# Optimization experiments

Hardware: AMD Instinct MI355X
Metric: run time of the kernel (lower is better)

The kernel has to match this reference:

```python
import jax, jax.numpy as jnp
import numpy as np

WS = 11
SIGMA = 1.5
L = 1.0  # val_range


def _gaussian_window(ws=WS, sigma=SIGMA):
    x = np.arange(ws, dtype=np.float64) - ws // 2
    g = np.exp(-(x ** 2) / (2.0 * sigma ** 2))
    g = g / g.sum()
    w2d = np.outer(g, g)
    return jnp.asarray(w2d, dtype=jnp.float32)  # [ws, ws]


def _depthwise_blur(x, w2d):
    # x: [B, C, H, W]; depthwise gaussian conv with SAME-style padding ws//2
    c = x.shape[1]
    kern = jnp.broadcast_to(w2d, (c, 1, WS, WS)).astype(x.dtype)  # OIHW, groups=C
    pad = WS // 2
    return jax.lax.conv_general_dilated(
        x, kern, window_strides=(1, 1), padding=[(pad, pad), (pad, pad)],
        dimension_numbers=('NCHW', 'OIHW', 'NCHW'), feature_group_count=c)


def setup_inputs() -> dict:
    key = jax.random.key(0)
    k1, k2 = jax.random.split(key)
    img1 = jax.random.uniform(k1, (32, 3, 512, 512), dtype=jnp.float32)
    img2 = jax.random.uniform(k2, (32, 3, 512, 512), dtype=jnp.float32)
    return {"img1": img1, "img2": img2}


def reference(img1, img2):
    w2d = _gaussian_window()
    mu1 = _depthwise_blur(img1, w2d)
    mu2 = _depthwise_blur(img2, w2d)
    mu1_sq = mu1 * mu1
    mu2_sq = mu2 * mu2
    mu1_mu2 = mu1 * mu2
    sigma1_sq = _depthwise_blur(img1 * img1, w2d) - mu1_sq
    sigma2_sq = _depthwise_blur(img2 * img2, w2d) - mu2_sq
    sigma12 = _depthwise_blur(img1 * img2, w2d) - mu1_mu2
    C1 = (0.01 * L) ** 2
    C2 = (0.03 * L) ** 2
    ssim_map = ((2.0 * mu1_mu2 + C1) * (2.0 * sigma12 + C2)) / (
        (mu1_sq + mu2_sq + C1) * (sigma1_sq + sigma2_sq + C2))
    return 1.0 - ssim_map.mean()
```

## Files before the change

kernel.cpp:

```cpp
#include <hip/hip_runtime.h>
#include <math.h>

typedef _Float16 f16;
typedef _Float16 f16x8 __attribute__((ext_vector_type(8)));
typedef _Float16 f16x4 __attribute__((ext_vector_type(4)));
typedef float f32x4 __attribute__((ext_vector_type(4)));

#define ROWS 88
#define NTHREADS 256

__device__ __forceinline__ float ssim_px(float m1, float m2, float mss, float m12) {
  const float C1 = 0.0001f, C2 = 0.0009f;
  const float mu1s = m1 * m1, mu2s = m2 * m2, mu12 = m1 * m2;
  const float num = (2.f * mu12 + C1) * (2.f * (m12 - mu12) + C2);
  const float den = (mu1s + mu2s + C1) * (mss - mu1s - mu2s + C2);
  return num * __builtin_amdgcn_rcpf(den);
}

__device__ __forceinline__ void h_phase(
    const float* __restrict__ p1, const float* __restrict__ p2,
    f16 (*si)[64][ROWS], bool masked,
    int gy0, int xb, int px, int n, int kg, const f16x8& Bh)
{
#pragma unroll
  for (int rg = 0; rg < 5; rg++) {
    const int rimg = gy0 + rg * 16 + n;
    float okf;
    size_t base;
    if (masked) {
      const bool octok = (xb >= 0) && (xb <= 504);
      const bool rok = (rimg >= 0) && (rimg < 512);
      okf = (rok && octok) ? 1.f : 0.f;
      const int rc = rok ? rimg : 0;
      const int xc = octok ? xb : 0;
      base = ((size_t)rc << 9) + (size_t)xc;
    } else {
      okf = 1.f;
      base = ((size_t)rimg << 9) + (size_t)xb;
    }
    const float4 a0 = *(const float4*)(p1 + base);
    const float4 a1 = *(const float4*)(p1 + base + 4);
    const float4 b0 = *(const float4*)(p2 + base);
    const float4 b1 = *(const float4*)(p2 + base + 4);
    const float av[8] = {a0.x, a0.y, a0.z, a0.w, a1.x, a1.y, a1.z, a1.w};
    const float bw[8] = {b0.x, b0.y, b0.z, b0.w, b1.x, b1.y, b1.z, b1.w};
    f16x8 fa, fb, fs, fp;
#pragma unroll
    for (int i = 0; i < 8; i++) {
      float ai = av[i], bi = bw[i];
      if (masked) { ai *= okf; bi *= okf; }
      fa[i] = (f16)ai;
      fb[i] = (f16)bi;
      fs[i] = (f16)fmaf(ai, ai, bi * bi);
      fp[i] = (f16)(ai * bi);
    }
    const f32x4 z = {0.f, 0.f, 0.f, 0.f};
    const f32x4 Da = __builtin_amdgcn_mfma_f32_16x16x32_f16(fa, Bh, z, 0, 0, 0);
    const f32x4 Db = __builtin_amdgcn_mfma_f32_16x16x32_f16(fb, Bh, z, 0, 0, 0);
    const f32x4 Ds = __builtin_amdgcn_mfma_f32_16x16x32_f16(fs, Bh, z, 0, 0, 0);
    const f32x4 Dp = __builtin_amdgcn_mfma_f32_16x16x32_f16(fp, Bh, z, 0, 0, 0);
    const int sr = rg * 16 + kg * 4;
    const f16x4 wa = {(f16)Da[0], (f16)Da[1], (f16)Da[2], (f16)Da[3]};
    const f16x4 wb = {(f16)Db[0], (f16)Db[1], (f16)Db[2], (f16)Db[3]};
    const f16x4 ws = {(f16)Ds[0], (f16)Ds[1], (f16)Ds[2], (f16)Ds[3]};
    const f16x4 wp = {(f16)Dp[0], (f16)Dp[1], (f16)Dp[2], (f16)Dp[3]};
    *(f16x4*)&si[0][px][sr] = wa;
    *(f16x4*)&si[1][px][sr] = wb;
    *(f16x4*)&si[2][px][sr] = ws;
    *(f16x4*)&si[3][px][sr] = wp;
  }
}

__global__ __launch_bounds__(NTHREADS) void ssim_main_kernel(
    const float* __restrict__ img1, const float* __restrict__ img2,
    float* __restrict__ partials, float norm, float cexp)
{
  __shared__ f16 si[4][64][ROWS];
  __shared__ float sred[4];

  const int tid = threadIdx.x;
  const int wv = tid >> 6, lane = tid & 63;
  const int n = lane & 15, kg = lane >> 4;

  int b = blockIdx.x;
  const int tx = b & 7; b >>= 3;
  const int ty = b & 7; b >>= 3;
  const float* __restrict__ p1 = img1 + (size_t)b * 262144;
  const float* __restrict__ p2 = img2 + (size_t)b * 262144;

  f16x8 Bh, Av;
#pragma unroll
  for (int i = 0; i < 8; i++) {
    const int k = 8 * kg + i;
    {
      const int idx = k - n - 3;
      const float d = (float)(idx - 5);
      const float val = norm * exp2f(cexp * d * d);
      Bh[i] = (idx >= 0 && idx <= 10) ? (f16)val : (f16)0.f;
    }
    {
      const int idx = k - n;
      const float d = (float)(idx - 5);
      const float val = norm * exp2f(cexp * d * d);
      Av[i] = (idx >= 0 && idx <= 10) ? (f16)val : (f16)0.f;
    }
  }

  const int X0 = tx * 64 + wv * 16;
  const int xb = X0 - 8 + 8 * kg;
  const int gy0 = ty * 64 - 5;
  const int px = wv * 16 + n;

  const bool interior = (tx >= 1) && (tx <= 6) && (ty >= 1) && (ty <= 6);
  if (interior)
    h_phase(p1, p2, si, false, gy0, xb, px, n, kg, Bh);
  else
    h_phase(p1, p2, si, true, gy0, xb, px, n, kg, Bh);
  __syncthreads();

  float acc4[4] = {0.f, 0.f, 0.f, 0.f};
#pragma unroll
  for (int og = 0; og < 4; og++) {
    const int srb = og * 16 + 8 * kg;
    const f16x8 Ba = *(const f16x8*)&si[0][px][srb];
    const f16x8 Bb = *(const f16x8*)&si[1][px][srb];
    const f16x8 Bs = *(const f16x8*)&si[2][px][srb];
    const f16x8 Bp = *(const f16x8*)&si[3][px][srb];
    const f32x4 z = {0.f, 0.f, 0.f, 0.f};
    const f32x4 Ma = __builtin_amdgcn_mfma_f32_16x16x32_f16(Av, Ba, z, 0, 0, 0);
    const f32x4 Mb = __builtin_amdgcn_mfma_f32_16x16x32_f16(Av, Bb, z, 0, 0, 0);
    const f32x4 Ms = __builtin_amdgcn_mfma_f32_16x16x32_f16(Av, Bs, z, 0, 0, 0);
    const f32x4 Mp = __builtin_amdgcn_mfma_f32_16x16x32_f16(Av, Bp, z, 0, 0, 0);
#pragma unroll
    for (int r = 0; r < 4; r++)
      acc4[r] += ssim_px(Ma[r], Mb[r], Ms[r], Mp[r]);
  }
  float accSum = (acc4[0] + acc4[1]) + (acc4[2] + acc4[3]);

  for (int off = 32; off > 0; off >>= 1)
    accSum += __shfl_down(accSum, off, 64);
  if (lane == 0) sred[wv] = accSum;
  __syncthreads();
  if (tid == 0)
    partials[blockIdx.x] = sred[0] + sred[1] + sred[2] + sred[3];
}

__global__ __launch_bounds__(256) void ssim_final_kernel(
    const float* __restrict__ partials, float* __restrict__ out,
    int n, double invN)
{
  __shared__ double sred[4];
  const int tid = threadIdx.x;
  double s = 0.0;
  for (int i = tid; i < n; i += 256) s += (double)partials[i];
  for (int off = 32; off > 0; off >>= 1)
    s += __shfl_down(s, off, 64);
  if ((tid & 63) == 0) sred[tid >> 6] = s;
  __syncthreads();
  if (tid == 0) {
    double tot = 0.0;
#pragma unroll
    for (int i = 0; i < 4; i++) tot += sred[i];
    out[0] = (float)(1.0 - tot * invN);
  }
}

extern "C" void kernel_launch(void* const* d_in, const int* in_sizes, int n_in,
                              void* d_out, int out_size, void* d_ws, size_t ws_size,
                              hipStream_t stream) {
  const float* img1 = (const float*)d_in[0];
  const float* img2 = (const float*)d_in[1];
  float* out = (float*)d_out;
  float* partials = (float*)d_ws;

  const int planes = in_sizes[0] / (512 * 512);
  const int nBlocks = planes * 8 * 8;

  double sum = 0.0;
  for (int i = 0; i < 11; i++) {
    const double x = (double)(i - 5);
    sum += exp(-(x * x) / 4.5);
  }
  const float norm = (float)(1.0 / sum);
  const float cexp = (float)(-1.0 / (4.5 * 0.6931471805599453));

  const double invN = 1.0 / (double)in_sizes[0];

  ssim_main_kernel<<<nBlocks, NTHREADS, 0, stream>>>(img1, img2, partials, norm, cexp);
  ssim_final_kernel<<<1, 256, 0, stream>>>(partials, out, nBlocks, invN);
}
```

Measured before the change: 80.01 us.

## Use three-slot ring buffer for horizontal results to cut LDS footprint

```diff
diff --git a/kernel.cpp b/kernel.cpp
--- a/kernel.cpp
+++ b/kernel.cpp
@@ -6,7 +6,7 @@
 typedef _Float16 f16x4 __attribute__((ext_vector_type(4)));
 typedef float f32x4 __attribute__((ext_vector_type(4)));
 
-#define ROWS 88
+#define RSTR 52
 #define NTHREADS 256
 
 __device__ __forceinline__ float ssim_px(float m1, float m2, float mss, float m12) {
@@ -17,65 +17,82 @@
   return num * __builtin_amdgcn_rcpf(den);
 }
 
-__device__ __forceinline__ void h_phase(
+template <bool MASKED>
+__device__ __forceinline__ void h_group(
     const float* __restrict__ p1, const float* __restrict__ p2,
-    f16 (*si)[64][ROWS], bool masked,
+    f16 (*si)[64][RSTR], int rg,
     int gy0, int xb, int px, int n, int kg, const f16x8& Bh)
 {
-#pragma unroll
-  for (int rg = 0; rg < 5; rg++) {
-    const int rimg = gy0 + rg * 16 + n;
-    float okf;
-    size_t base;
-    if (masked) {
-      const bool octok = (xb >= 0) && (xb <= 504);
-      const bool rok = (rimg >= 0) && (rimg < 512);
-      okf = (rok && octok) ? 1.f : 0.f;
-      const int rc = rok ? rimg : 0;
-      const int xc = octok ? xb : 0;
-      base = ((size_t)rc << 9) + (size_t)xc;
-    } else {
-      okf = 1.f;
-      base = ((size_t)rimg << 9) + (size_t)xb;
-    }
-    const float4 a0 = *(const float4*)(p1 + base);
-    const float4 a1 = *(const float4*)(p1 + base + 4);
-    const float4 b0 = *(const float4*)(p2 + base);
-    const float4 b1 = *(const float4*)(p2 + base + 4);
-    const float av[8] = {a0.x, a0.y, a0.z, a0.w, a1.x, a1.y, a1.z, a1.w};
-    const float bw[8] = {b0.x, b0.y, b0.z, b0.w, b1.x, b1.y, b1.z, b1.w};
-    f16x8 fa, fb, fs, fp;
-#pragma unroll
-    for (int i = 0; i < 8; i++) {
-      float ai = av[i], bi = bw[i];
-      if (masked) { ai *= okf; bi *= okf; }
-      fa[i] = (f16)ai;
-      fb[i] = (f16)bi;
-      fs[i] = (f16)fmaf(ai, ai, bi * bi);
-      fp[i] = (f16)(ai * bi);
-    }
-    const f32x4 z = {0.f, 0.f, 0.f, 0.f};
-    const f32x4 Da = __builtin_amdgcn_mfma_f32_16x16x32_f16(fa, Bh, z, 0, 0, 0);
-    const f32x4 Db = __builtin_amdgcn_mfma_f32_16x16x32_f16(fb, Bh, z, 0, 0, 0);
-    const f32x4 Ds = __builtin_amdgcn_mfma_f32_16x16x32_f16(fs, Bh, z, 0, 0, 0);
-    const f32x4 Dp = __builtin_amdgcn_mfma_f32_16x16x32_f16(fp, Bh, z, 0, 0, 0);
-    const int sr = rg * 16 + kg * 4;
-    const f16x4 wa = {(f16)Da[0], (f16)Da[1], (f16)Da[2], (f16)Da[3]};
-    const f16x4 wb = {(f16)Db[0], (f16)Db[1], (f16)Db[2], (f16)Db[3]};
-    const f16x4 ws = {(f16)Ds[0], (f16)Ds[1], (f16)Ds[2], (f16)Ds[3]};
-    const f16x4 wp = {(f16)Dp[0], (f16)Dp[1], (f16)Dp[2], (f16)Dp[3]};
-    *(f16x4*)&si[0][px][sr] = wa;
-    *(f16x4*)&si[1][px][sr] = wb;
-    *(f16x4*)&si[2][px][sr] = ws;
-    *(f16x4*)&si[3][px][sr] = wp;
-  }
+  const int rimg = gy0 + rg * 16 + n;
+  float okf;
+  size_t base;
+  if (MASKED) {
+    const bool octok = (xb >= 0) && (xb <= 504);
+    const bool rok = (rimg >= 0) && (rimg < 512);
+    okf = (rok && octok) ? 1.f : 0.f;
+    const int rc = rok ? rimg : 0;
+    const int xc = octok ? xb : 0;
+    base = ((size_t)rc << 9) + (size_t)xc;
+  } else {
+    okf = 1.f;
+    base = ((size_t)rimg << 9) + (size_t)xb;
+  }
+  const float4 a0 = *(const float4*)(p1 + base);
+  const float4 a1 = *(const float4*)(p1 + base + 4);
+  const float4 b0 = *(const float4*)(p2 + base);
+  const float4 b1 = *(const float4*)(p2 + base + 4);
+  const float av[8] = {a0.x, a0.y, a0.z, a0.w, a1.x, a1.y, a1.z, a1.w};
+  const float bw[8] = {b0.x, b0.y, b0.z, b0.w, b1.x, b1.y, b1.z, b1.w};
+  f16x8 fa, fb, fs, fp;
+#pragma unroll
+  for (int i = 0; i < 8; i++) {
+    float ai = av[i], bi = bw[i];
+    if (MASKED) { ai *= okf; bi *= okf; }
+    fa[i] = (f16)ai;
+    fb[i] = (f16)bi;
+    fs[i] = (f16)fmaf(ai, ai, bi * bi);
+    fp[i] = (f16)(ai * bi);
+  }
+  const f32x4 z = {0.f, 0.f, 0.f, 0.f};
+  const f32x4 Da = __builtin_amdgcn_mfma_f32_16x16x32_f16(fa, Bh, z, 0, 0, 0);
+  const f32x4 Db = __builtin_amdgcn_mfma_f32_16x16x32_f16(fb, Bh, z, 0, 0, 0);
+  const f32x4 Ds = __builtin_amdgcn_mfma_f32_16x16x32_f16(fs, Bh, z, 0, 0, 0);
+  const f32x4 Dp = __builtin_amdgcn_mfma_f32_16x16x32_f16(fp, Bh, z, 0, 0, 0);
+  const int sr = (rg % 3) * 16 + kg * 4;
+  const f16x4 wa = {(f16)Da[0], (f16)Da[1], (f16)Da[2], (f16)Da[3]};
+  const f16x4 wb = {(f16)Db[0], (f16)Db[1], (f16)Db[2], (f16)Db[3]};
+  const f16x4 ws = {(f16)Ds[0], (f16)Ds[1], (f16)Ds[2], (f16)Ds[3]};
+  const f16x4 wp = {(f16)Dp[0], (f16)Dp[1], (f16)Dp[2], (f16)Dp[3]};
+  *(f16x4*)&si[0][px][sr] = wa;
+  *(f16x4*)&si[1][px][sr] = wb;
+  *(f16x4*)&si[2][px][sr] = ws;
+  *(f16x4*)&si[3][px][sr] = wp;
+}
+
+__device__ __forceinline__ void v_group(
+    f16 (*si)[64][RSTR], int og, int px, int kg, const f16x8& Av, float acc4[4])
+{
+  int srb = og * 16 + 8 * kg;
+  srb = srb >= 48 ? srb - 48 : srb;
+  const f16x8 Ba = *(const f16x8*)&si[0][px][srb];
+  const f16x8 Bb = *(const f16x8*)&si[1][px][srb];
+  const f16x8 Bs = *(const f16x8*)&si[2][px][srb];
+  const f16x8 Bp = *(const f16x8*)&si[3][px][srb];
+  const f32x4 z = {0.f, 0.f, 0.f, 0.f};
+  const f32x4 Ma = __builtin_amdgcn_mfma_f32_16x16x32_f16(Av, Ba, z, 0, 0, 0);
+  const f32x4 Mb = __builtin_amdgcn_mfma_f32_16x16x32_f16(Av, Bb, z, 0, 0, 0);
+  const f32x4 Ms = __builtin_amdgcn_mfma_f32_16x16x32_f16(Av, Bs, z, 0, 0, 0);
+  const f32x4 Mp = __builtin_amdgcn_mfma_f32_16x16x32_f16(Av, Bp, z, 0, 0, 0);
+#pragma unroll
+  for (int r = 0; r < 4; r++)
+    acc4[r] += ssim_px(Ma[r], Mb[r], Ms[r], Mp[r]);
 }
 
 __global__ __launch_bounds__(NTHREADS) void ssim_main_kernel(
     const float* __restrict__ img1, const float* __restrict__ img2,
     float* __restrict__ partials, float norm, float cexp)
 {
-  __shared__ f16 si[4][64][ROWS];
+  __shared__ f16 si[4][64][RSTR];
   __shared__ float sred[4];
 
   const int tid = threadIdx.x;
@@ -112,29 +129,39 @@
   const int px = wv * 16 + n;
 
   const bool interior = (tx >= 1) && (tx <= 6) && (ty >= 1) && (ty <= 6);
-  if (interior)
-    h_phase(p1, p2, si, false, gy0, xb, px, n, kg, Bh);
-  else
-    h_phase(p1, p2, si, true, gy0, xb, px, n, kg, Bh);
-  __syncthreads();
-
   float acc4[4] = {0.f, 0.f, 0.f, 0.f};
-#pragma unroll
-  for (int og = 0; og < 4; og++) {
-    const int srb = og * 16 + 8 * kg;
-    const f16x8 Ba = *(const f16x8*)&si[0][px][srb];
-    const f16x8 Bb = *(const f16x8*)&si[1][px][srb];
-    const f16x8 Bs = *(const f16x8*)&si[2][px][srb];
-    const f16x8 Bp = *(const f16x8*)&si[3][px][srb];
-    const f32x4 z = {0.f, 0.f, 0.f, 0.f};
-    const f32x4 Ma = __builtin_amdgcn_mfma_f32_16x16x32_f16(Av, Ba, z, 0, 0, 0);
-    const f32x4 Mb = __builtin_amdgcn_mfma_f32_16x16x32_f16(Av, Bb, z, 0, 0, 0);
-    const f32x4 Ms = __builtin_amdgcn_mfma_f32_16x16x32_f16(Av, Bs, z, 0, 0, 0);
-    const f32x4 Mp = __builtin_amdgcn_mfma_f32_16x16x32_f16(Av, Bp, z, 0, 0, 0);
-#pragma unroll
-    for (int r = 0; r < 4; r++)
-      acc4[r] += ssim_px(Ma[r], Mb[r], Ms[r], Mp[r]);
-  }
+
+  if (interior) {
+#pragma unroll
+    for (int rg = 0; rg < 3; rg++)
+      h_group<false>(p1, p2, si, rg, gy0, xb, px, n, kg, Bh);
+  } else {
+#pragma unroll
+    for (int rg = 0; rg < 3; rg++)
+      h_group<true>(p1, p2, si, rg, gy0, xb, px, n, kg, Bh);
+  }
+  __syncthreads();
+
+#pragma unroll
+  for (int og = 0; og < 2; og++)
+    v_group(si, og, px, kg, Av, acc4);
+  __syncthreads();
+
+  if (interior) {
+#pragma unroll
+    for (int rg = 3; rg < 5; rg++)
+      h_group<false>(p1, p2, si, rg, gy0, xb, px, n, kg, Bh);
+  } else {
+#pragma unroll
+    for (int rg = 3; rg < 5; rg++)
+      h_group<true>(p1, p2, si, rg, gy0, xb, px, n, kg, Bh);
+  }
+  __syncthreads();
+
+#pragma unroll
+  for (int og = 2; og < 4; og++)
+    v_group(si, og, px, kg, Av, acc4);
+
   float accSum = (acc4[0] + acc4[1]) + (acc4[2] + acc4[3]);
 
   for (int off = 32; off > 0; off >>= 1)
```

Result: slower. 86.37 us (+8.0%).
